# Kernel optimization log

Hardware: AMD Instinct MI355X
Metric: run time of the kernel (lower is better)

The kernel has to match this reference:

```python
import jax, jax.numpy as jnp
import numpy as np

B, W, H, F = 4096, 64, 64, 1024
SHRINK = 0.25
LR, B1, B2, EPS, WD = 0.1, 0.9, 0.999, 1e-8, 1e-2  # torch AdamW defaults except lr
STEPS = 50


def setup_inputs() -> dict:
    key = jax.random.key(0)
    k1, k2 = jax.random.split(key)
    images = jax.random.uniform(k1, (B, W, H), dtype=jnp.float32)
    filters = jax.random.uniform(k2, (W, H, F), dtype=jnp.float32)
    # normalize_weights(): unit L2 norm per filter column over flattened pixels
    Phi = filters.reshape(-1, F)
    norms = jnp.maximum(jnp.linalg.norm(Phi, axis=0, keepdims=True), 1e-12)
    filters = (Phi / norms).reshape(W, H, F)
    return {"images": images, "filters": filters}


def _activations(images, filters):
    Fd = filters.shape[-1]
    Phi = filters.reshape(-1, Fd)                      # [W*H, F]
    x = images.reshape(images.shape[0], -1)            # [B, W*H]
    excite = x @ Phi                                   # [B, F]
    inhibit = Phi.T @ Phi                              # [F, F]
    u0 = jnp.zeros_like(excite)

    def step(carry, t):
        u, m, v = carry
        act = jax.nn.relu(u - SHRINK)
        du = -u + excite - (act @ inhibit - act)
        g = -du                                        # u.grad = -u_grad
        # AdamW: decoupled weight decay then Adam update with bias correction
        u = u * (1.0 - LR * WD)
        m = B1 * m + (1.0 - B1) * g
        v = B2 * v + (1.0 - B2) * g * g
        mhat = m / (1.0 - B1 ** t)
        vhat = v / (1.0 - B2 ** t)
        u = u - LR * mhat / (jnp.sqrt(vhat) + EPS)
        return (u, m, v), None

    ts = jnp.arange(1, STEPS + 1, dtype=jnp.float32)
    (u, _, _), _ = jax.lax.scan(step, (u0, u0, u0), ts)
    return jax.nn.relu(u - SHRINK)


def reference(images, filters):
    acts = _activations(images, filters)               # [B, F]
    # matmul(filters, acts.T): [W,H,B] -> swapaxes -> [B, W, H]
    recon = jnp.einsum('whf,bf->bwh', filters, acts)
    return (recon, acts)
```

## Files before the change

kernel.cpp:

```cpp
#include <hip/hip_runtime.h>
#include <math.h>


typedef __bf16 bf16_t;
typedef __bf16 bf16x8 __attribute__((ext_vector_type(8)));
typedef __bf16 bf16x4 __attribute__((ext_vector_type(4)));
typedef float f32x4 __attribute__((ext_vector_type(4)));

__device__ __forceinline__ void async_ld16(const void* g, void* l) {
    __builtin_amdgcn_global_load_lds(
        (const __attribute__((address_space(1))) void*)g,
        (__attribute__((address_space(3))) void*)l, 16, 0, 0);
}

__device__ __forceinline__ float ag_read(const float& a_) {
    float v;
    asm("v_accvgpr_read_b32 %0, %1" : "=v"(v) : "a"(a_));
    return v;
}
__device__ __forceinline__ void ag_write(float& a_, float v) {
    asm("v_accvgpr_write_b32 %0, %1" : "=a"(a_) : "v"(v));
}

__global__ void cvt_bf16(const float* __restrict__ x, bf16_t* __restrict__ y, long n) {
    long i = ((long)blockIdx.x * blockDim.x + threadIdx.x) * 4;
    if (i + 3 < n) {
        float4 f = *(const float4*)(x + i);
        bf16x4 o = { (bf16_t)f.x, (bf16_t)f.y, (bf16_t)f.z, (bf16_t)f.w };
        *(bf16x4*)(y + i) = o;
    }
}

__global__ void transpose_cvt(const float* __restrict__ src, bf16_t* __restrict__ dst) {
    __shared__ float tile[32][33];
    const int f0 = blockIdx.x * 32;
    const int p0 = blockIdx.y * 32;
    const int tx = threadIdx.x, ty = threadIdx.y;
    for (int r = ty; r < 32; r += 8)
        tile[r][tx] = src[(size_t)(p0 + r) * 1024 + f0 + tx];
    __syncthreads();
    for (int r = ty; r < 32; r += 8)
        dst[(size_t)(f0 + r) * 4096 + p0 + tx] = (bf16_t)tile[tx][r];
}

template<int MODE>
__global__ __launch_bounds__(256) void gemm_bt(
    const bf16_t* __restrict__ A, const bf16_t* __restrict__ BT,
    int M, int N, int K,
    float* __restrict__ Cf, bf16_t* __restrict__ Cb)
{
    __shared__ bf16_t As[128 * 32];
    __shared__ bf16_t Bs[128 * 32];
    const int tid  = threadIdx.x;
    const int n0   = blockIdx.x * 128;
    const int m0   = blockIdx.y * 128;
    const int wave = tid >> 6;
    const int lane = tid & 63;
    const int wm   = (wave >> 1) * 64;
    const int wn   = (wave & 1) * 64;
    const int r0   = tid >> 2;
    const int kc   = (tid & 3) * 8;
    const int lr   = lane >> 4;
    const int lc   = lane & 15;

    f32x4 acc[4][4] = {};
    const size_t arow0 = (size_t)(m0 + r0) * K;
    const size_t arow1 = (size_t)(m0 + 64 + r0) * K;
    const size_t brow0 = (size_t)(n0 + r0) * K;
    const size_t brow1 = (size_t)(n0 + 64 + r0) * K;

    for (int k0 = 0; k0 < K; k0 += 32) {
        async_ld16(A + arow0 + k0 + kc, &As[(size_t)tid * 8]);
        async_ld16(A + arow1 + k0 + kc, &As[(size_t)(tid + 256) * 8]);
        async_ld16(BT + brow0 + k0 + kc, &Bs[(size_t)tid * 8]);
        async_ld16(BT + brow1 + k0 + kc, &Bs[(size_t)(tid + 256) * 8]);
        __syncthreads();
        bf16x8 af[4], bv[4];
#pragma unroll
        for (int i = 0; i < 4; ++i) {
            af[i] = *(const bf16x8*)&As[(wm + i * 16 + lc) * 32 + lr * 8];
            bv[i] = *(const bf16x8*)&Bs[(wn + i * 16 + lc) * 32 + lr * 8];
        }
#pragma unroll
        for (int i = 0; i < 4; ++i)
#pragma unroll
            for (int j = 0; j < 4; ++j)
                acc[i][j] = __builtin_amdgcn_mfma_f32_16x16x32_bf16(af[i], bv[j], acc[i][j], 0, 0, 0);
        __syncthreads();
    }

#pragma unroll
    for (int i = 0; i < 4; ++i)
#pragma unroll
        for (int t = 0; t < 4; ++t) {
            const int row = m0 + wm + i * 16 + lr * 4 + t;
#pragma unroll
            for (int j = 0; j < 4; ++j) {
                const int col = n0 + wn + j * 16 + lc;
                if constexpr (MODE == 0) {
                    Cf[(size_t)row * N + col] = acc[i][j][t];
                } else {
                    Cb[(size_t)(((row >> 5) << 10) + col) * 32 + (row & 31)] =
                        (bf16_t)acc[i][j][t];
                }
            }
        }
}

__global__ __launch_bounds__(1024) __attribute__((amdgpu_waves_per_eu(4, 4)))
void lca_persistent(
    const bf16_t* __restrict__ Gblk, const float* __restrict__ excite,
    float* __restrict__ actsf, bf16_t* __restrict__ actbf)
{
    __shared__ bf16_t act[16 * 1024];
    __shared__ float  exs[16 * 1024];
    const int tid  = threadIdx.x;
    const int m0   = blockIdx.x * 16;
    const int wave = tid >> 6;
    const int lane = tid & 63;
    const int lr   = lane >> 4;
    const int lc   = lane & 15;
    const int wn   = wave * 64;

    for (int i = tid; i < 16 * 1024 / 8; i += 1024) {
        bf16x8 z = {};
        *(bf16x8*)&act[i * 8] = z;
    }
    {
        const float* esrc = excite + (size_t)m0 * 1024;
        for (int i = tid; i < 16 * 1024 / 4; i += 1024)
            *(f32x4*)&exs[i * 4] = *(const f32x4*)(esrc + (size_t)i * 4);
    }
    __syncthreads();

    float Ua[4][4], Ma[4][4], Va[4][4];
#pragma unroll
    for (int j = 0; j < 4; ++j)
#pragma unroll
        for (int t = 0; t < 4; ++t) {
            ag_write(Ua[j][t], 0.0f);
            ag_write(Ma[j][t], 0.0f);
            ag_write(Va[j][t], 0.0f);
        }

    const int aoff = lc * 1024;
    const int lcx  = lc & 7;
    const bf16_t* gpt = Gblk + (((wn + lc) << 5) + lr * 8);

    const float lrate = 0.1f, b1 = 0.9f, b2 = 0.999f, eps = 1e-8f;
    const float wdmul = 1.0f - lrate * 1e-2f;
    float pb1 = 1.0f, pb2 = 1.0f;

    for (int step = 1; step <= 50; ++step) {
        pb1 *= b1; pb2 *= b2;
        const float inv1 = 1.0f / (1.0f - pb1);
        const float inv2 = 1.0f / (1.0f - pb2);

        f32x4 acc[4] = {};
#pragma unroll 1
        for (int kcb = 0; kcb < 32; ++kcb) {
            const int unit = kcb * 4 + lr;
            const bf16x8 a = *(const bf16x8*)&act[aoff + ((unit ^ lcx) << 3)];
            const bf16_t* gp = gpt + ((size_t)kcb << 15);
            bf16x8 b0 = *(const bf16x8*)(gp);
            bf16x8 b1v = *(const bf16x8*)(gp + 512);
            bf16x8 b2v = *(const bf16x8*)(gp + 1024);
            bf16x8 b3 = *(const bf16x8*)(gp + 1536);
            acc[0] = __builtin_amdgcn_mfma_f32_16x16x32_bf16(a, b0,  acc[0], 0, 0, 0);
            acc[1] = __builtin_amdgcn_mfma_f32_16x16x32_bf16(a, b1v, acc[1], 0, 0, 0);
            acc[2] = __builtin_amdgcn_mfma_f32_16x16x32_bf16(a, b2v, acc[2], 0, 0, 0);
            acc[3] = __builtin_amdgcn_mfma_f32_16x16x32_bf16(a, b3,  acc[3], 0, 0, 0);
        }
        __syncthreads();

#pragma unroll
        for (int j = 0; j < 4; ++j)
#pragma unroll
            for (int t = 0; t < 4; ++t) {
                const int row = lr * 4 + t;
                const int col = wn + j * 16 + lc;
                const float ex   = exs[row * 1024 + col];
                const float uold = ag_read(Ua[j][t]);
                const float mold = ag_read(Ma[j][t]);
                const float vold = ag_read(Va[j][t]);
                const float aold = fmaxf(uold - 0.25f, 0.0f);
                const float g    = uold - ex + acc[j][t] - aold;
                const float mn   = b1 * mold + (1.0f - b1) * g;
                const float vn   = b2 * vold + (1.0f - b2) * g * g;
                float un = uold * wdmul;
                un -= lrate * (mn * inv1) / (sqrtf(vn * inv2) + eps);
                ag_write(Ua[j][t], un);
                ag_write(Ma[j][t], mn);
                ag_write(Va[j][t], vn);
                const float an = fmaxf(un - 0.25f, 0.0f);
                const int su = (col >> 3) ^ (row & 7);
                act[row * 1024 + (su << 3) + (col & 7)] = (bf16_t)an;
                if (step == 50) {
                    actsf[(size_t)(m0 + row) * 1024 + col] = an;
                    actbf[(size_t)(m0 + row) * 1024 + col] = (bf16_t)an;
                }
            }
        __syncthreads();
    }
}

extern "C" void kernel_launch(void* const* d_in, const int* in_sizes, int n_in,
                              void* d_out, int out_size, void* d_ws, size_t ws_size,
                              hipStream_t stream)
{
    const float* images  = (const float*)d_in[0];
    const float* filters = (const float*)d_in[1];
    float* out = (float*)d_out;

    constexpr int B = 4096, P = 4096, F = 1024;
    constexpr size_t BF = (size_t)B * F;
    constexpr size_t BP = (size_t)B * P;

    bf16_t* xbf    = (bf16_t*)out;
    float*  excite = out + 2 * BF;
    float*  actsf  = out + BP;

    bf16_t* w0    = (bf16_t*)d_ws;
    bf16_t* Gblk  = w0 + BF;
    bf16_t* phibf = w0 + BF + BF / 4;

    dim3 blk(256);
    cvt_bf16<<<(unsigned)(BP / 4 / 256), blk, 0, stream>>>(images, xbf, (long)BP);
    transpose_cvt<<<dim3(F / 32, P / 32), dim3(32, 8), 0, stream>>>(filters, w0);
    gemm_bt<0><<<dim3(F / 128, B / 128), blk, 0, stream>>>(
        xbf, w0, B, F, P, excite, nullptr);
    gemm_bt<3><<<dim3(F / 128, F / 128), blk, 0, stream>>>(
        w0, w0, F, F, P, nullptr, Gblk);
    lca_persistent<<<dim3(B / 16), dim3(1024), 0, stream>>>(Gblk, excite, actsf, w0);
    cvt_bf16<<<(unsigned)(BF / 4 / 256), blk, 0, stream>>>(filters, phibf, (long)BF);
    gemm_bt<0><<<dim3(P / 128, B / 128), blk, 0, stream>>>(
        w0, phibf, B, P, F, out, nullptr);
}
```

Baseline: 2.128 ms.

## Software-pipeline Gram operand loads in LCA loop and relayout excite in LDS

The inner k-loop of the persistent LCA kernel now prefetches the next iteration's activation fragment from LDS and the next two Gram-matrix fragments from global memory, interleaved with the current MFMAs, to hide load latency. Excite is stored in LDS in a per-thread f32x4 layout so each thread reads its four values with one vector load instead of scattered scalar reads. The final activation store is moved out of the step loop, removing the per-step branch. This adds register pressure under a fixed waves-per-EU constraint, which could cause spills.

Measured after the change: 2.105 ms. Within noise of the previous version (-1.1%).

```diff
diff --git a/kernel.cpp b/kernel.cpp
--- a/kernel.cpp
+++ b/kernel.cpp
@@ -113,7 +113,7 @@
     float* __restrict__ actsf, bf16_t* __restrict__ actbf)
 {
     __shared__ bf16_t act[16 * 1024];
-    __shared__ float  exs[16 * 1024];
+    __shared__ f32x4  exsv[4096];
     const int tid  = threadIdx.x;
     const int m0   = blockIdx.x * 16;
     const int wave = tid >> 6;
@@ -126,10 +126,13 @@
         bf16x8 z = {};
         *(bf16x8*)&act[i * 8] = z;
     }
-    {
-        const float* esrc = excite + (size_t)m0 * 1024;
-        for (int i = tid; i < 16 * 1024 / 4; i += 1024)
-            *(f32x4*)&exs[i * 4] = *(const f32x4*)(esrc + (size_t)i * 4);
+#pragma unroll
+    for (int j = 0; j < 4; ++j) {
+        f32x4 e;
+#pragma unroll
+        for (int t = 0; t < 4; ++t)
+            e[t] = excite[(size_t)(m0 + lr * 4 + t) * 1024 + wn + j * 16 + lc];
+        exsv[j * 1024 + tid] = e;
     }
     __syncthreads();
 
@@ -157,34 +160,44 @@
         const float inv2 = 1.0f / (1.0f - pb2);
 
         f32x4 acc[4] = {};
+        {
+            const bf16_t* gp = gpt;
+            bf16x8 a_cur = *(const bf16x8*)&act[aoff + ((lr ^ lcx) << 3)];
+            bf16x8 p0 = *(const bf16x8*)(gp);
+            bf16x8 p1 = *(const bf16x8*)(gp + 512);
+            bf16x8 a_nxt, n0, n1;
 #pragma unroll 1
-        for (int kcb = 0; kcb < 32; ++kcb) {
-            const int unit = kcb * 4 + lr;
-            const bf16x8 a = *(const bf16x8*)&act[aoff + ((unit ^ lcx) << 3)];
-            const bf16_t* gp = gpt + ((size_t)kcb << 15);
-            bf16x8 b0 = *(const bf16x8*)(gp);
-            bf16x8 b1v = *(const bf16x8*)(gp + 512);
-            bf16x8 b2v = *(const bf16x8*)(gp + 1024);
-            bf16x8 b3 = *(const bf16x8*)(gp + 1536);
-            acc[0] = __builtin_amdgcn_mfma_f32_16x16x32_bf16(a, b0,  acc[0], 0, 0, 0);
-            acc[1] = __builtin_amdgcn_mfma_f32_16x16x32_bf16(a, b1v, acc[1], 0, 0, 0);
-            acc[2] = __builtin_amdgcn_mfma_f32_16x16x32_bf16(a, b2v, acc[2], 0, 0, 0);
-            acc[3] = __builtin_amdgcn_mfma_f32_16x16x32_bf16(a, b3,  acc[3], 0, 0, 0);
-        }
-        __syncthreads();
-
-#pragma unroll
-        for (int j = 0; j < 4; ++j)
+            for (int kcb = 0; kcb < 32; ++kcb) {
+                bf16x8 q0 = *(const bf16x8*)(gp + 1024);
+                bf16x8 q1 = *(const bf16x8*)(gp + 1536);
+                acc[0] = __builtin_amdgcn_mfma_f32_16x16x32_bf16(a_cur, p0, acc[0], 0, 0, 0);
+                acc[1] = __builtin_amdgcn_mfma_f32_16x16x32_bf16(a_cur, p1, acc[1], 0, 0, 0);
+                if (kcb < 31) {
+                    const int unit = (kcb + 1) * 4 + lr;
+                    a_nxt = *(const bf16x8*)&act[aoff + ((unit ^ lcx) << 3)];
+                    gp += (size_t)1 << 15;
+                    n0 = *(const bf16x8*)(gp);
+                    n1 = *(const bf16x8*)(gp + 512);
+                }
+                acc[2] = __builtin_amdgcn_mfma_f32_16x16x32_bf16(a_cur, q0, acc[2], 0, 0, 0);
+                acc[3] = __builtin_amdgcn_mfma_f32_16x16x32_bf16(a_cur, q1, acc[3], 0, 0, 0);
+                a_cur = a_nxt; p0 = n0; p1 = n1;
+            }
+        }
+        __syncthreads();
+
+#pragma unroll
+        for (int j = 0; j < 4; ++j) {
+            const f32x4 ex4 = exsv[j * 1024 + tid];
 #pragma unroll
             for (int t = 0; t < 4; ++t) {
                 const int row = lr * 4 + t;
                 const int col = wn + j * 16 + lc;
-                const float ex   = exs[row * 1024 + col];
                 const float uold = ag_read(Ua[j][t]);
                 const float mold = ag_read(Ma[j][t]);
                 const float vold = ag_read(Va[j][t]);
                 const float aold = fmaxf(uold - 0.25f, 0.0f);
-                const float g    = uold - ex + acc[j][t] - aold;
+                const float g    = uold - ex4[t] + acc[j][t] - aold;
                 const float mn   = b1 * mold + (1.0f - b1) * g;
                 const float vn   = b2 * vold + (1.0f - b2) * g * g;
                 float un = uold * wdmul;
@@ -195,13 +208,21 @@
                 const float an = fmaxf(un - 0.25f, 0.0f);
                 const int su = (col >> 3) ^ (row & 7);
                 act[row * 1024 + (su << 3) + (col & 7)] = (bf16_t)an;
-                if (step == 50) {
-                    actsf[(size_t)(m0 + row) * 1024 + col] = an;
-                    actbf[(size_t)(m0 + row) * 1024 + col] = (bf16_t)an;
-                }
             }
-        __syncthreads();
-    }
+        }
+        __syncthreads();
+    }
+
+#pragma unroll
+    for (int j = 0; j < 4; ++j)
+#pragma unroll
+        for (int t = 0; t < 4; ++t) {
+            const int row = lr * 4 + t;
+            const int col = wn + j * 16 + lc;
+            const float an = fmaxf(ag_read(Ua[j][t]) - 0.25f, 0.0f);
+            actsf[(size_t)(m0 + row) * 1024 + col] = an;
+            actbf[(size_t)(m0 + row) * 1024 + col] = (bf16_t)an;
+        }
 }
 
 extern "C" void kernel_launch(void* const* d_in, const int* in_sizes, int n_in,
```
